# Optimization experiments

Measured on AMD Instinct MI355X. Metric: run time of the kernel, lower is better.

The kernel has to match this reference:

```python
import jax, jax.numpy as jnp
import numpy as np

N = 50000        # nodes
E = 800000       # edges (avg degree 16)
HIDDEN = 256
HEADS = 8
HEAD_DIM = HIDDEN // HEADS


def _linear_params(key, fan_in, fan_out):
    k1, k2 = jax.random.split(key)
    s = 1.0 / np.sqrt(fan_in)
    W = jax.random.uniform(k1, (fan_in, fan_out), jnp.float32, -s, s)
    b = jax.random.uniform(k2, (fan_out,), jnp.float32, -s, s)
    return W, b


def setup_inputs() -> dict:
    key = jax.random.key(0)
    ks = jax.random.split(key, 7)
    h = jax.random.normal(ks[0], (N, HIDDEN), jnp.float32)
    # sparse adjacency nonzeros: row = destination node, col = source node
    row = jnp.sort(jax.random.randint(ks[1], (E,), 0, N))
    col = jax.random.randint(ks[2], (E,), 0, N)
    Wq, bq = _linear_params(ks[3], HIDDEN, HIDDEN)
    Wk, bk = _linear_params(ks[4], HIDDEN, HIDDEN)
    Wv, bv = _linear_params(ks[5], HIDDEN, HIDDEN)
    Wo, bo = _linear_params(ks[6], HIDDEN, HIDDEN)
    return dict(h=h, row=row, col=col, Wq=Wq, bq=bq, Wk=Wk, bk=bk,
                Wv=Wv, bv=bv, Wo=Wo, bo=bo)


def reference(h, row, col, Wq, bq, Wk, bk, Wv, bv, Wo, bo):
    n = h.shape[0]
    scaling = HEAD_DIM ** (-0.5)
    q = ((h @ Wq + bq).reshape(n, HEADS, HEAD_DIM)) * scaling
    k = (h @ Wk + bk).reshape(n, HEADS, HEAD_DIM)
    v = (h @ Wv + bv).reshape(n, HEADS, HEAD_DIM)

    # bsddmm: per-edge, per-head sampled dot product q[dst] . k[src] -> [E, H]
    s = jnp.einsum('ehd,ehd->eh', q[row], k[col])

    # sparse row-wise softmax over each destination node's incoming edges
    m = jax.ops.segment_max(s, row, num_segments=n)          # [N, H]
    p = jnp.exp(s - m[row])                                   # [E, H]
    denom = jax.ops.segment_sum(p, row, num_segments=n)      # [N, H]
    attn = p / denom[row]                                     # [E, H]

    # bspmm: out[dst] = sum over incoming edges attn * v[src] -> [N, H, D]
    out = jax.ops.segment_sum(attn[:, :, None] * v[col], row, num_segments=n)
    return out.reshape(n, HIDDEN) @ Wo + bo
```

## Files before the change

### kernel.cpp

```cpp
#include <hip/hip_runtime.h>
#include <math.h>


typedef __attribute__((ext_vector_type(8))) short bf16x8;
typedef __attribute__((ext_vector_type(4))) float f32x4;
typedef __attribute__((ext_vector_type(2))) float f32x2;

__device__ __forceinline__ ushort f2bf(float f) {
    uint u = __float_as_uint(f);
    u += 0x7fffu + ((u >> 16) & 1u);
    return (ushort)(u >> 16);
}
__device__ __forceinline__ float bflo(uint u) { return __uint_as_float(u << 16); }
__device__ __forceinline__ float bfhi(uint u) { return __uint_as_float(u & 0xffff0000u); }

__device__ __forceinline__ uchar f2fp8(float f) {
    return (uchar)(__builtin_amdgcn_cvt_pk_fp8_f32(f, f, 0, false) & 0xff);
}
__device__ __forceinline__ void fp8x4_to_f32(uint u, float* f) {
    f32x2 lo = __builtin_amdgcn_cvt_pk_f32_fp8(u, false);
    f32x2 hi = __builtin_amdgcn_cvt_pk_f32_fp8(u, true);
    f[0] = lo[0]; f[1] = lo[1]; f[2] = hi[0]; f[3] = hi[1];
}

__device__ __forceinline__ void load_lds16(const void* g, void* l) {
    __builtin_amdgcn_global_load_lds(
        (const __attribute__((address_space(1))) void*)g,
        (__attribute__((address_space(3))) void*)l, 16, 0, 0);
}

__global__ __launch_bounds__(256) void convert_bf16(
    const float* __restrict__ in, ushort* __restrict__ out, size_t nelem)
{
    size_t i = ((size_t)blockIdx.x * 256 + threadIdx.x) * 4;
    if (i >= nelem) return;
    float4 v = *(const float4*)(in + i);
    *(ushort4*)(out + i) = make_ushort4(f2bf(v.x), f2bf(v.y), f2bf(v.z), f2bf(v.w));
}

__global__ __launch_bounds__(256) void prep_w(
    const float* __restrict__ Wq, const float* __restrict__ Wk,
    const float* __restrict__ Wv, const float* __restrict__ Wo,
    const float* __restrict__ bq, const float* __restrict__ bk,
    const float* __restrict__ bv,
    ushort* __restrict__ Wall, ushort* __restrict__ Wot,
    float* __restrict__ ball)
{
    int m = blockIdx.y;
    if (blockIdx.x < 256) {
        int idx = blockIdx.x * 256 + threadIdx.x;
        int k = idx >> 8, nn = idx & 255;
        if (m < 3) {
            const float* W = m == 0 ? Wq : (m == 1 ? Wk : Wv);
            Wall[((size_t)m * 256 + nn) * 256 + k] = f2bf(W[idx]);
        } else {
            Wot[nn * 256 + k] = f2bf(Wo[idx]);
        }
    } else if (m < 3) {
        int i = threadIdx.x;
        ball[m * 256 + i] = (m == 0 ? bq : (m == 1 ? bk : bv))[i];
    }
}

template<int MODE>
__global__ __launch_bounds__(256) void gemm_mfma_lds(
    const ushort* __restrict__ A, const ushort* __restrict__ Wt,
    const float* __restrict__ bias, ushort* __restrict__ qb,
    uchar* __restrict__ kv, float* __restrict__ outf, int n, float scale)
{
    __shared__ ushort SH[2 * 128 * 64];
    ushort* As = SH;
    ushort* Bs = SH + 128 * 64;

    const int nwg = gridDim.x * gridDim.y;
    const int orig = blockIdx.y * gridDim.x + blockIdx.x;
    const int xcd = orig & 7, rnd = orig >> 3;
    const int q8 = nwg >> 3, r8 = nwg & 7;
    const int wgid = (xcd < r8 ? xcd * (q8 + 1) : r8 * (q8 + 1) + (xcd - r8) * q8) + rnd;
    const int tx = wgid % gridDim.x;
    const int ty = wgid / gridDim.x;

    const int tid = threadIdx.x;
    const int lane = tid & 63;
    const int wave = tid >> 6;
    const int col0 = tx * 128;
    const int row0 = ty * 128;
    const int fr = lane & 15;
    const int kg = lane >> 4;
    const int wr = (wave >> 1) * 64;
    const int wc = (wave & 1) * 64;

    f32x4 acc[4][4] = {};

    const int srow = tid >> 3;
    const int sc8 = tid & 7;

    for (int kt = 0; kt < 4; ++kt) {
        #pragma unroll
        for (int it = 0; it < 4; ++it) {
            int r = srow + it * 32;
            int chunk = sc8 ^ (r & 7);
            int ar = row0 + r; ar = ar < n ? ar : n - 1;
            load_lds16((const char*)A + (size_t)ar * 512 + kt * 128 + chunk * 16,
                       (char*)As + (it * 256 + tid) * 16);
            load_lds16((const char*)Wt + (size_t)(col0 + r) * 512 + kt * 128 + chunk * 16,
                       (char*)Bs + (it * 256 + tid) * 16);
        }
        __syncthreads();

        #pragma unroll
        for (int ks = 0; ks < 2; ++ks) {
            bf16x8 a[4], b[4];
            #pragma unroll
            for (int i = 0; i < 4; ++i) {
                int r = wr + i * 16 + fr;
                int chunk = (ks * 4 + kg) ^ (r & 7);
                a[i] = *(const bf16x8*)((const char*)As + r * 128 + chunk * 16);
            }
            #pragma unroll
            for (int j = 0; j < 4; ++j) {
                int c = wc + j * 16 + fr;
                int chunk = (ks * 4 + kg) ^ (c & 7);
                b[j] = *(const bf16x8*)((const char*)Bs + c * 128 + chunk * 16);
            }
            #pragma unroll
            for (int i = 0; i < 4; ++i)
                #pragma unroll
                for (int j = 0; j < 4; ++j)
                    acc[i][j] = __builtin_amdgcn_mfma_f32_16x16x32_bf16(
                        a[i], b[j], acc[i][j], 0, 0, 0);
        }
        __syncthreads();
    }

    if constexpr (MODE == 1) {
        #pragma unroll
        for (int j = 0; j < 4; ++j) {
            int gcol = col0 + wc + j * 16 + fr;
            float bj = bias[gcol];
            #pragma unroll
            for (int i = 0; i < 4; ++i) {
                #pragma unroll
                for (int r = 0; r < 4; ++r) {
                    int grow = row0 + wr + i * 16 + kg * 4 + r;
                    if (grow >= n) continue;
                    outf[(size_t)grow * 256 + gcol] = acc[i][j][r] + bj;
                }
            }
        }
        return;
    }

    char* sb = (char*)SH;
    const bool isf8 = (col0 >= 256 && col0 < 512);
    const float sc = (col0 < 256) ? scale : 1.f;

    #pragma unroll
    for (int j = 0; j < 4; ++j) {
        int cw = wc + j * 16 + fr;
        float bj = bias[col0 + cw];
        #pragma unroll
        for (int i = 0; i < 4; ++i) {
            #pragma unroll
            for (int r = 0; r < 4; ++r) {
                int lrow = wr + i * 16 + kg * 4 + r;
                float val = (acc[i][j][r] + bj) * sc;
                if (isf8) {
                    int u = cw >> 4;
                    sb[lrow * 128 + ((u ^ (lrow & 7)) << 4) + (cw & 15)] = f2fp8(val);
                } else {
                    int u = cw >> 3;
                    *(ushort*)(sb + lrow * 256 + ((u ^ (lrow & 7)) << 4) +
                               ((cw & 7) << 1)) = f2bf(val);
                }
            }
        }
    }
    __syncthreads();

    if (isf8) {
        int seg = col0 - 256;
        #pragma unroll
        for (int pass = 0; pass < 4; ++pass) {
            int g = pass * 256 + tid;
            int lrow = g >> 3, u = g & 7;
            uint4 d = *(const uint4*)(sb + lrow * 128 + ((u ^ (lrow & 7)) << 4));
            int grow = row0 + lrow;
            if (grow < n)
                *(uint4*)((char*)kv + (size_t)grow * 768 + seg + u * 16) = d;
        }
    } else {
        char* dst; size_t stride; int seg;
        if (col0 < 256) { dst = (char*)qb; stride = 512; seg = col0 * 2; }
        else            { dst = (char*)kv; stride = 768; seg = 256 + (col0 - 512) * 2; }
        #pragma unroll
        for (int pass = 0; pass < 8; ++pass) {
            int g = pass * 256 + tid;
            int lrow = g >> 4, u = g & 15;
            uint4 d = *(const uint4*)(sb + lrow * 256 + ((u ^ (lrow & 7)) << 4));
            int grow = row0 + lrow;
            if (grow < n)
                *(uint4*)(dst + (size_t)grow * stride + seg + u * 16) = d;
        }
    }
}

__global__ __launch_bounds__(256) void build_row_ptr(
    const int* __restrict__ row, int* __restrict__ row_ptr, int n, int E)
{
    int i = blockIdx.x * 256 + threadIdx.x;
    if (i > n) return;
    int lo = 0, hi = E;
    while (lo < hi) {
        int mid = (lo + hi) >> 1;
        if (row[mid] < i) lo = mid + 1; else hi = mid;
    }
    row_ptr[i] = lo;
}

__global__ __launch_bounds__(256) void fused_attn(
    const ushort* __restrict__ qb, const uchar* __restrict__ kv,
    const int* __restrict__ col, const int* __restrict__ row_ptr,
    ushort* __restrict__ agg, int n)
{
    int node = blockIdx.x * 4 + (threadIdx.x >> 6);
    if (node >= n) return;
    int lane = threadIdx.x & 63;
    int p0 = row_ptr[node], p1 = row_ptr[node + 1];

    const int slot = lane >> 4;
    const int l16 = lane & 15;
    const int qoff = l16 * 32;

    float qf[16];
    {
        const char* qbp = (const char*)qb + (size_t)node * 512 + qoff;
        uint4 q0 = *(const uint4*)qbp;
        uint4 q1 = *(const uint4*)(qbp + 16);
        qf[0] = bflo(q0.x); qf[1] = bfhi(q0.x);
        qf[2] = bflo(q0.y); qf[3] = bfhi(q0.y);
        qf[4] = bflo(q0.z); qf[5] = bfhi(q0.z);
        qf[6] = bflo(q0.w); qf[7] = bfhi(q0.w);
        qf[8] = bflo(q1.x); qf[9] = bfhi(q1.x);
        qf[10] = bflo(q1.y); qf[11] = bfhi(q1.y);
        qf[12] = bflo(q1.z); qf[13] = bfhi(q1.z);
        qf[14] = bflo(q1.w); qf[15] = bfhi(q1.w);
    }

    float denom = 0.f;
    float acc[16] = {};

#define ISSUE(IDX, K, V0, V1)                                                  \
    do {                                                                       \
        int src_ = __shfl(cl, (IDX));                                          \
        const char* b_ = (const char*)kv + (size_t)src_ * 768;                 \
        K  = *(const uint4*)(b_ + l16 * 16);                                   \
        V0 = *(const uint4*)(b_ + 256 + l16 * 32);                             \
        V1 = *(const uint4*)(b_ + 272 + l16 * 32);                             \
    } while (0)

#define CONSUME(VALID, K, V0, V1)                                              \
    do {                                                                       \
        float kf_[16];                                                         \
        fp8x4_to_f32(K.x, kf_); fp8x4_to_f32(K.y, kf_ + 4);                    \
        fp8x4_to_f32(K.z, kf_ + 8); fp8x4_to_f32(K.w, kf_ + 12);               \
        float sp_ = 0.f;                                                       \
        _Pragma("unroll")                                                      \
        for (int i_ = 0; i_ < 16; ++i_) sp_ = fmaf(qf[i_], kf_[i_], sp_);      \
        float s_ = sp_ + __shfl_xor(sp_, 1);                                   \
        float p_ = (VALID) ? __expf(s_) : 0.f;                                 \
        denom += p_;                                                           \
        acc[0]  = fmaf(p_, bflo(V0.x), acc[0]);                                \
        acc[1]  = fmaf(p_, bfhi(V0.x), acc[1]);                                \
        acc[2]  = fmaf(p_, bflo(V0.y), acc[2]);                                \
        acc[3]  = fmaf(p_, bfhi(V0.y), acc[3]);                                \
        acc[4]  = fmaf(p_, bflo(V0.z), acc[4]);                                \
        acc[5]  = fmaf(p_, bfhi(V0.z), acc[5]);                                \
        acc[6]  = fmaf(p_, bflo(V0.w), acc[6]);                                \
        acc[7]  = fmaf(p_, bfhi(V0.w), acc[7]);                                \
        acc[8]  = fmaf(p_, bflo(V1.x), acc[8]);                                \
        acc[9]  = fmaf(p_, bfhi(V1.x), acc[9]);                                \
        acc[10] = fmaf(p_, bflo(V1.y), acc[10]);                               \
        acc[11] = fmaf(p_, bfhi(V1.y), acc[11]);                               \
        acc[12] = fmaf(p_, bflo(V1.z), acc[12]);                               \
        acc[13] = fmaf(p_, bfhi(V1.z), acc[13]);                               \
        acc[14] = fmaf(p_, bflo(V1.w), acc[14]);                               \
        acc[15] = fmaf(p_, bfhi(V1.w), acc[15]);                               \
    } while (0)

    for (int bbase = p0; bbase < p1; bbase += 64) {
        int bd = min(64, p1 - bbase);
        int cl = (lane < bd) ? col[bbase + lane] : 0;
        int nch = (bd + 3) >> 2;

        uint4 kA, vA0, vA1, kB, vB0, vB1;
        ISSUE(slot, kA, vA0, vA1);
        int c = 0;
        for (;;) {
            if (c + 1 < nch) ISSUE((c + 1) * 4 + slot, kB, vB0, vB1);
            CONSUME(c * 4 + slot < bd, kA, vA0, vA1);
            if (++c >= nch) break;
            if (c + 1 < nch) ISSUE((c + 1) * 4 + slot, kA, vA0, vA1);
            CONSUME(c * 4 + slot < bd, kB, vB0, vB1);
            if (++c >= nch) break;
        }
    }
#undef ISSUE
#undef CONSUME

    #pragma unroll
    for (int i = 0; i < 16; ++i) {
        acc[i] += __shfl_xor(acc[i], 16);
        acc[i] += __shfl_xor(acc[i], 32);
    }
    denom += __shfl_xor(denom, 16);
    denom += __shfl_xor(denom, 32);

    if (slot == 0) {
        float inv = denom > 0.f ? 1.f / denom : 0.f;
        uint o[8];
        #pragma unroll
        for (int i = 0; i < 8; ++i)
            o[i] = (uint)f2bf(acc[2 * i] * inv) |
                   ((uint)f2bf(acc[2 * i + 1] * inv) << 16);
        char* ob = (char*)agg + (size_t)node * 512 + qoff;
        *(uint4*)ob        = make_uint4(o[0], o[1], o[2], o[3]);
        *(uint4*)(ob + 16) = make_uint4(o[4], o[5], o[6], o[7]);
    }
}

extern "C" void kernel_launch(void* const* d_in, const int* in_sizes, int n_in,
                              void* d_out, int out_size, void* d_ws, size_t ws_size,
                              hipStream_t stream)
{
    const float* h  = (const float*)d_in[0];
    const int*   row = (const int*)d_in[1];
    const int*   col = (const int*)d_in[2];
    const float* Wq = (const float*)d_in[3];
    const float* bq = (const float*)d_in[4];
    const float* Wk = (const float*)d_in[5];
    const float* bk = (const float*)d_in[6];
    const float* Wv = (const float*)d_in[7];
    const float* bv = (const float*)d_in[8];
    const float* Wo = (const float*)d_in[9];
    const float* bo = (const float*)d_in[10];
    float* out = (float*)d_out;

    const int n = in_sizes[0] / 256;
    const int E = in_sizes[1];
    const size_t NC = (size_t)n * 256;

    char* base = (char*)d_ws;
    ushort* qbb  = (ushort*)(base);
    uchar*  kv   = (uchar*)(base + NC * 2);
    ushort* hb   = (ushort*)(base + NC * 2 + (size_t)n * 768);
    ushort* aggb = (ushort*)(base + NC * 4 + (size_t)n * 768);
    ushort* Wall = (ushort*)(base + NC * 6 + (size_t)n * 768);
    ushort* Wot  = Wall + 768 * 256;
    float*  ball = (float*)(Wot + 65536);
    int* row_ptr = (int*)(ball + 768);

    const float scaling = 0.17677669529663687f;

    dim3 blk(256);
    convert_bf16<<<dim3((int)((NC / 4 + 255) / 256)), blk, 0, stream>>>(h, hb, NC);
    prep_w<<<dim3(257, 4), blk, 0, stream>>>(Wq, Wk, Wv, Wo, bq, bk, bv,
                                             Wall, Wot, ball);
    build_row_ptr<<<dim3((n + 256) / 256), blk, 0, stream>>>(row, row_ptr, n, E);

    const int mtiles = (n + 127) / 128;
    gemm_mfma_lds<0><<<dim3(6, mtiles), blk, 0, stream>>>(
        hb, Wall, ball, qbb, kv, nullptr, n, scaling);

    fused_attn<<<dim3((n + 3) / 4), blk, 0, stream>>>(
        qbb, kv, col, row_ptr, aggb, n);

    gemm_mfma_lds<1><<<dim3(2, mtiles), blk, 0, stream>>>(
        aggb, Wot, bo, nullptr, nullptr, out, n, 1.f);
}
```

Before: 175.7 us.

## Fuse fp32-to-bf16 conversion into QKV GEMM with resident A tile, merge prep launches

The QKV projection now loads h as fp32 directly, converts it to bf16 into a swizzled LDS tile covering the full K dimension for 64 rows, and loops over all six output column tiles inside one block. This removes the separate conversion kernel and its intermediate bf16 buffer round trip through memory. The row_ptr binary search is folded into the weight prep kernel as an extra grid row, saving a launch. In exchange there are fewer, heavier blocks with larger LDS use, and no double buffering of the weight tiles.

```diff
diff --git a/kernel.cpp b/kernel.cpp
--- a/kernel.cpp
+++ b/kernel.cpp
@@ -29,24 +29,27 @@
         (__attribute__((address_space(3))) void*)l, 16, 0, 0);
 }
 
-__global__ __launch_bounds__(256) void convert_bf16(
-    const float* __restrict__ in, ushort* __restrict__ out, size_t nelem)
-{
-    size_t i = ((size_t)blockIdx.x * 256 + threadIdx.x) * 4;
-    if (i >= nelem) return;
-    float4 v = *(const float4*)(in + i);
-    *(ushort4*)(out + i) = make_ushort4(f2bf(v.x), f2bf(v.y), f2bf(v.z), f2bf(v.w));
-}
-
-__global__ __launch_bounds__(256) void prep_w(
+__global__ __launch_bounds__(256) void prep(
     const float* __restrict__ Wq, const float* __restrict__ Wk,
     const float* __restrict__ Wv, const float* __restrict__ Wo,
     const float* __restrict__ bq, const float* __restrict__ bk,
     const float* __restrict__ bv,
+    const int* __restrict__ row, int* __restrict__ row_ptr, int n, int E,
     ushort* __restrict__ Wall, ushort* __restrict__ Wot,
     float* __restrict__ ball)
 {
     int m = blockIdx.y;
+    if (m == 4) {
+        int i = blockIdx.x * 256 + threadIdx.x;
+        if (i > n) return;
+        int lo = 0, hi = E;
+        while (lo < hi) {
+            int mid = (lo + hi) >> 1;
+            if (row[mid] < i) lo = mid + 1; else hi = mid;
+        }
+        row_ptr[i] = lo;
+        return;
+    }
     if (blockIdx.x < 256) {
         int idx = blockIdx.x * 256 + threadIdx.x;
         int k = idx >> 8, nn = idx & 255;
@@ -62,15 +65,139 @@
     }
 }
 
-template<int MODE>
-__global__ __launch_bounds__(256) void gemm_mfma_lds(
+__global__ __launch_bounds__(256) void gemm_qkv(
+    const float* __restrict__ h, const ushort* __restrict__ Wall,
+    const float* __restrict__ ball, ushort* __restrict__ qb,
+    uchar* __restrict__ kv, int n, float scale)
+{
+    __shared__ ushort As[64 * 256];
+    __shared__ ushort Bs[128 * 64];
+
+    const int tid = threadIdx.x;
+    const int lane = tid & 63;
+    const int wave = tid >> 6;
+    const int row0 = blockIdx.x * 64;
+
+    #pragma unroll 4
+    for (int j = 0; j < 16; ++j) {
+        int r = j * 4 + wave;
+        int src_r = row0 + r; if (src_r >= n) src_r = n - 1;
+        float4 f = *(const float4*)((const char*)h + (size_t)src_r * 1024 + lane * 16);
+        uint lo = (uint)f2bf(f.x) | ((uint)f2bf(f.y) << 16);
+        uint hi = (uint)f2bf(f.z) | ((uint)f2bf(f.w) << 16);
+        int addr = r * 512 + (((lane >> 1) ^ (r & 7)) << 4) + ((lane & 1) << 3);
+        *(uint2*)((char*)As + addr) = make_uint2(lo, hi);
+    }
+
+    const int fr = lane & 15;
+    const int kg = lane >> 4;
+    const int wr = (wave >> 1) * 32;
+    const int wc = (wave & 1) * 64;
+
+    for (int ct = 0; ct < 6; ++ct) {
+        f32x4 acc[2][4] = {};
+
+        for (int kt = 0; kt < 4; ++kt) {
+            #pragma unroll
+            for (int it = 0; it < 4; ++it) {
+                int r = (tid >> 3) + it * 32;
+                int chunk = (tid & 7) ^ (r & 7);
+                load_lds16((const char*)Wall + (size_t)(ct * 128 + r) * 512 +
+                               kt * 128 + chunk * 16,
+                           (char*)Bs + (it * 256 + tid) * 16);
+            }
+            __syncthreads();
+
+            #pragma unroll
+            for (int ks = 0; ks < 2; ++ks) {
+                bf16x8 a[2], b[4];
+                #pragma unroll
+                for (int i = 0; i < 2; ++i) {
+                    int r = wr + i * 16 + fr;
+                    int c16 = kt * 8 + ks * 4 + kg;
+                    a[i] = *(const bf16x8*)((const char*)As + r * 512 +
+                                            ((c16 ^ (r & 7)) << 4));
+                }
+                #pragma unroll
+                for (int jj = 0; jj < 4; ++jj) {
+                    int rb = wc + jj * 16 + fr;
+                    int chunk = (ks * 4 + kg) ^ (rb & 7);
+                    b[jj] = *(const bf16x8*)((const char*)Bs + rb * 128 + chunk * 16);
+                }
+                #pragma unroll
+                for (int i = 0; i < 2; ++i)
+                    #pragma unroll
+                    for (int jj = 0; jj < 4; ++jj)
+                        acc[i][jj] = __builtin_amdgcn_mfma_f32_16x16x32_bf16(
+                            a[i], b[jj], acc[i][jj], 0, 0, 0);
+            }
+            __syncthreads();
+        }
+
+        const bool isf8 = (ct == 2 || ct == 3);
+        const float sc = (ct < 2) ? scale : 1.f;
+        char* sb = (char*)Bs;
+
+        #pragma unroll
+        for (int jj = 0; jj < 4; ++jj) {
+            int cw = wc + jj * 16 + fr;
+            float bj = ball[ct * 128 + cw];
+            #pragma unroll
+            for (int i = 0; i < 2; ++i) {
+                #pragma unroll
+                for (int r2 = 0; r2 < 4; ++r2) {
+                    int lrow = wr + i * 16 + kg * 4 + r2;
+                    float val = (acc[i][jj][r2] + bj) * sc;
+                    if (isf8) {
+                        int u = cw >> 4;
+                        sb[lrow * 128 + ((u ^ (lrow & 7)) << 4) + (cw & 15)] =
+                            f2fp8(val);
+                    } else {
+                        int u = cw >> 3;
+                        *(ushort*)(sb + lrow * 256 + ((u ^ (lrow & 7)) << 4) +
+                                   ((cw & 7) << 1)) = f2bf(val);
+                    }
+                }
+            }
+        }
+        __syncthreads();
+
+        if (isf8) {
+            #pragma unroll
+            for (int cp = 0; cp < 2; ++cp) {
+                int g = cp * 256 + tid;
+                int lrow = g >> 3, u = g & 7;
+                uint4 d = *(const uint4*)(sb + lrow * 128 + ((u ^ (lrow & 7)) << 4));
+                int grow = row0 + lrow;
+                if (grow < n)
+                    *(uint4*)((char*)kv + (size_t)grow * 768 + (ct - 2) * 128 +
+                              u * 16) = d;
+            }
+        } else {
+            #pragma unroll
+            for (int cp = 0; cp < 4; ++cp) {
+                int g = cp * 256 + tid;
+                int lrow = g >> 4, u = g & 15;
+                uint4 d = *(const uint4*)(sb + lrow * 256 + ((u ^ (lrow & 7)) << 4));
+                int grow = row0 + lrow;
+                if (grow >= n) continue;
+                if (ct < 2)
+                    *(uint4*)((char*)qb + (size_t)grow * 512 + ct * 256 + u * 16) = d;
+                else
+                    *(uint4*)((char*)kv + (size_t)grow * 768 + 256 +
+                              (ct - 4) * 256 + u * 16) = d;
+            }
+        }
+        __syncthreads();
+    }
+}
+
+__global__ __launch_bounds__(256) void gemm_out(
     const ushort* __restrict__ A, const ushort* __restrict__ Wt,
-    const float* __restrict__ bias, ushort* __restrict__ qb,
-    uchar* __restrict__ kv, float* __restrict__ outf, int n, float scale)
+    const float* __restrict__ bias, float* __restrict__ outf, int n)
 {
-    __shared__ ushort SH[2 * 128 * 64];
-    ushort* As = SH;
-    ushort* Bs = SH + 128 * 64;
+    __shared__ ushort As[128 * 64];
+    __shared__ ushort Bs[128 * 64];
 
     const int nwg = gridDim.x * gridDim.y;
     const int orig = blockIdx.y * gridDim.x + blockIdx.x;
@@ -133,89 +260,20 @@
         __syncthreads();
     }
 
-    if constexpr (MODE == 1) {
-        #pragma unroll
-        for (int j = 0; j < 4; ++j) {
-            int gcol = col0 + wc + j * 16 + fr;
-            float bj = bias[gcol];
-            #pragma unroll
-            for (int i = 0; i < 4; ++i) {
-                #pragma unroll
-                for (int r = 0; r < 4; ++r) {
-                    int grow = row0 + wr + i * 16 + kg * 4 + r;
-                    if (grow >= n) continue;
-                    outf[(size_t)grow * 256 + gcol] = acc[i][j][r] + bj;
-                }
-            }
-        }
-        return;
-    }
-
-    char* sb = (char*)SH;
-    const bool isf8 = (col0 >= 256 && col0 < 512);
-    const float sc = (col0 < 256) ? scale : 1.f;
-
     #pragma unroll
     for (int j = 0; j < 4; ++j) {
-        int cw = wc + j * 16 + fr;
-        float bj = bias[col0 + cw];
+        int gcol = col0 + wc + j * 16 + fr;
+        float bj = bias[gcol];
         #pragma unroll
         for (int i = 0; i < 4; ++i) {
             #pragma unroll
             for (int r = 0; r < 4; ++r) {
-                int lrow = wr + i * 16 + kg * 4 + r;
-                float val = (acc[i][j][r] + bj) * sc;
-                if (isf8) {
-                    int u = cw >> 4;
-                    sb[lrow * 128 + ((u ^ (lrow & 7)) << 4) + (cw & 15)] = f2fp8(val);
-                } else {
-                    int u = cw >> 3;
-                    *(ushort*)(sb + lrow * 256 + ((u ^ (lrow & 7)) << 4) +
-                               ((cw & 7) << 1)) = f2bf(val);
-                }
-            }
-        }
-    }
-    __syncthreads();
-
-    if (isf8) {
-        int seg = col0 - 256;
-        #pragma unroll
-        for (int pass = 0; pass < 4; ++pass) {
-            int g = pass * 256 + tid;
-            int lrow = g >> 3, u = g & 7;
-            uint4 d = *(const uint4*)(sb + lrow * 128 + ((u ^ (lrow & 7)) << 4));
-            int grow = row0 + lrow;
-            if (grow < n)
-                *(uint4*)((char*)kv + (size_t)grow * 768 + seg + u * 16) = d;
-        }
-    } else {
-        char* dst; size_t stride; int seg;
-        if (col0 < 256) { dst = (char*)qb; stride = 512; seg = col0 * 2; }
-        else            { dst = (char*)kv; stride = 768; seg = 256 + (col0 - 512) * 2; }
-        #pragma unroll
-        for (int pass = 0; pass < 8; ++pass) {
-            int g = pass * 256 + tid;
-            int lrow = g >> 4, u = g & 15;
-            uint4 d = *(const uint4*)(sb + lrow * 256 + ((u ^ (lrow & 7)) << 4));
-            int grow = row0 + lrow;
-            if (grow < n)
-                *(uint4*)(dst + (size_t)grow * stride + seg + u * 16) = d;
-        }
-    }
-}
-
-__global__ __launch_bounds__(256) void build_row_ptr(
-    const int* __restrict__ row, int* __restrict__ row_ptr, int n, int E)
-{
-    int i = blockIdx.x * 256 + threadIdx.x;
-    if (i > n) return;
-    int lo = 0, hi = E;
-    while (lo < hi) {
-        int mid = (lo + hi) >> 1;
-        if (row[mid] < i) lo = mid + 1; else hi = mid;
-    }
-    row_ptr[i] = lo;
+                int grow = row0 + wr + i * 16 + kg * 4 + r;
+                if (grow >= n) continue;
+                outf[(size_t)grow * 256 + gcol] = acc[i][j][r] + bj;
+            }
+        }
+    }
 }
 
 __global__ __launch_bounds__(256) void fused_attn(
@@ -353,9 +411,8 @@
     char* base = (char*)d_ws;
     ushort* qbb  = (ushort*)(base);
     uchar*  kv   = (uchar*)(base + NC * 2);
-    ushort* hb   = (ushort*)(base + NC * 2 + (size_t)n * 768);
-    ushort* aggb = (ushort*)(base + NC * 4 + (size_t)n * 768);
-    ushort* Wall = (ushort*)(base + NC * 6 + (size_t)n * 768);
+    ushort* aggb = (ushort*)(base + NC * 2 + (size_t)n * 768);
+    ushort* Wall = (ushort*)(base + NC * 4 + (size_t)n * 768);
     ushort* Wot  = Wall + 768 * 256;
     float*  ball = (float*)(Wot + 65536);
     int* row_ptr = (int*)(ball + 768);
@@ -363,18 +420,16 @@
     const float scaling = 0.17677669529663687f;
 
     dim3 blk(256);
-    convert_bf16<<<dim3((int)((NC / 4 + 255) / 256)), blk, 0, stream>>>(h, hb, NC);
-    prep_w<<<dim3(257, 4), blk, 0, stream>>>(Wq, Wk, Wv, Wo, bq, bk, bv,
-                                             Wall, Wot, ball);
-    build_row_ptr<<<dim3((n + 256) / 256), blk, 0, stream>>>(row, row_ptr, n, E);
-
-    const int mtiles = (n + 127) / 128;
-    gemm_mfma_lds<0><<<dim3(6, mtiles), blk, 0, stream>>>(
-        hb, Wall, ball, qbb, kv, nullptr, n, scaling);
+    prep<<<dim3(257, 5), blk, 0, stream>>>(Wq, Wk, Wv, Wo, bq, bk, bv,
+                                           row, row_ptr, n, E,
+                                           Wall, Wot, ball);
+
+    gemm_qkv<<<dim3((n + 63) / 64), blk, 0, stream>>>(
+        h, Wall, ball, qbb, kv, n, scaling);
 
     fused_attn<<<dim3((n + 3) / 4), blk, 0, stream>>>(
         qbb, kv, col, row_ptr, aggb, n);
 
-    gemm_mfma_lds<1><<<dim3(2, mtiles), blk, 0, stream>>>(
-        aggb, Wot, bo, nullptr, nullptr, out, n, 1.f);
-}
+    gemm_out<<<dim3(2, (n + 127) / 128), blk, 0, stream>>>(
+        aggb, Wot, bo, out, n);
+}
```

New measurement: 178.8 us. About the same (+1.7%).

## Quantize V to per-head int8 with scales and merge row_ptr build into prep

Applied to the files above, without the earlier changes.

Stores V as unsigned 8-bit values with a per-node, per-head float scale (absmax/127, offset 128) instead of bf16. The per-row K/V record in the gathered buffer shrinks from 768 to 544 bytes. The attention kernel gathers one 16-byte V load plus a scale per edge, accumulates on the offset bytes, and corrects the offset at the end with a running sum. The row_ptr binary search is also folded into the weight-prep kernel to save one launch. The lower V precision adds accuracy risk and a few extra conversion ALU ops per edge.

```diff
diff --git a/kernel.cpp b/kernel.cpp
--- a/kernel.cpp
+++ b/kernel.cpp
@@ -38,15 +38,27 @@
     *(ushort4*)(out + i) = make_ushort4(f2bf(v.x), f2bf(v.y), f2bf(v.z), f2bf(v.w));
 }
 
-__global__ __launch_bounds__(256) void prep_w(
+__global__ __launch_bounds__(256) void prep(
     const float* __restrict__ Wq, const float* __restrict__ Wk,
     const float* __restrict__ Wv, const float* __restrict__ Wo,
     const float* __restrict__ bq, const float* __restrict__ bk,
     const float* __restrict__ bv,
+    const int* __restrict__ row, int* __restrict__ row_ptr, int n, int E,
     ushort* __restrict__ Wall, ushort* __restrict__ Wot,
     float* __restrict__ ball)
 {
     int m = blockIdx.y;
+    if (m == 4) {
+        int i = blockIdx.x * 256 + threadIdx.x;
+        if (i > n) return;
+        int lo = 0, hi = E;
+        while (lo < hi) {
+            int mid = (lo + hi) >> 1;
+            if (row[mid] < i) lo = mid + 1; else hi = mid;
+        }
+        row_ptr[i] = lo;
+        return;
+    }
     if (blockIdx.x < 256) {
         int idx = blockIdx.x * 256 + threadIdx.x;
         int k = idx >> 8, nn = idx & 255;
@@ -153,6 +165,7 @@
 
     char* sb = (char*)SH;
     const bool isf8 = (col0 >= 256 && col0 < 512);
+    const bool isv  = (col0 >= 512);
     const float sc = (col0 < 256) ? scale : 1.f;
 
     #pragma unroll
@@ -162,9 +175,9 @@
         #pragma unroll
         for (int i = 0; i < 4; ++i) {
             #pragma unroll
-            for (int r = 0; r < 4; ++r) {
-                int lrow = wr + i * 16 + kg * 4 + r;
-                float val = (acc[i][j][r] + bj) * sc;
+            for (int r2 = 0; r2 < 4; ++r2) {
+                int lrow = wr + i * 16 + kg * 4 + r2;
+                float val = (acc[i][j][r2] + bj) * sc;
                 if (isf8) {
                     int u = cw >> 4;
                     sb[lrow * 128 + ((u ^ (lrow & 7)) << 4) + (cw & 15)] = f2fp8(val);
@@ -187,12 +200,48 @@
             uint4 d = *(const uint4*)(sb + lrow * 128 + ((u ^ (lrow & 7)) << 4));
             int grow = row0 + lrow;
             if (grow < n)
-                *(uint4*)((char*)kv + (size_t)grow * 768 + seg + u * 16) = d;
+                *(uint4*)((char*)kv + (size_t)grow * 544 + seg + u * 16) = d;
+        }
+    } else if (isv) {
+        int vseg = col0 - 512;
+        #pragma unroll
+        for (int pass = 0; pass < 2; ++pass) {
+            int t = pass * 256 + tid;
+            int lrow = t >> 2, hh = t & 3;
+            float vals[32];
+            #pragma unroll
+            for (int uu = 0; uu < 4; ++uu) {
+                int u = hh * 4 + uu;
+                uint4 d = *(const uint4*)(sb + lrow * 256 + ((u ^ (lrow & 7)) << 4));
+                vals[uu*8+0] = bflo(d.x); vals[uu*8+1] = bfhi(d.x);
+                vals[uu*8+2] = bflo(d.y); vals[uu*8+3] = bfhi(d.y);
+                vals[uu*8+4] = bflo(d.z); vals[uu*8+5] = bfhi(d.z);
+                vals[uu*8+6] = bflo(d.w); vals[uu*8+7] = bfhi(d.w);
+            }
+            float mx = 0.f;
+            #pragma unroll
+            for (int i = 0; i < 32; ++i) mx = fmaxf(mx, fabsf(vals[i]));
+            float inv = mx > 0.f ? 127.f / mx : 0.f;
+            float scl = mx > 0.f ? mx * (1.f / 127.f) : 0.f;
+            uint pk[8];
+            #pragma unroll
+            for (int w = 0; w < 8; ++w) {
+                uint b0 = (uint)(__float2int_rn(vals[w*4+0] * inv) + 128);
+                uint b1 = (uint)(__float2int_rn(vals[w*4+1] * inv) + 128);
+                uint b2 = (uint)(__float2int_rn(vals[w*4+2] * inv) + 128);
+                uint b3 = (uint)(__float2int_rn(vals[w*4+3] * inv) + 128);
+                pk[w] = b0 | (b1 << 8) | (b2 << 16) | (b3 << 24);
+            }
+            int grow = row0 + lrow;
+            if (grow < n) {
+                char* dst = (char*)kv + (size_t)grow * 544 + 256 + vseg + hh * 32;
+                *(uint4*)dst        = make_uint4(pk[0], pk[1], pk[2], pk[3]);
+                *(uint4*)(dst + 16) = make_uint4(pk[4], pk[5], pk[6], pk[7]);
+                *(float*)((char*)kv + (size_t)grow * 544 + 512 +
+                          ((vseg >> 5) + hh) * 4) = scl;
+            }
         }
     } else {
-        char* dst; size_t stride; int seg;
-        if (col0 < 256) { dst = (char*)qb; stride = 512; seg = col0 * 2; }
-        else            { dst = (char*)kv; stride = 768; seg = 256 + (col0 - 512) * 2; }
         #pragma unroll
         for (int pass = 0; pass < 8; ++pass) {
             int g = pass * 256 + tid;
@@ -200,22 +249,9 @@
             uint4 d = *(const uint4*)(sb + lrow * 256 + ((u ^ (lrow & 7)) << 4));
             int grow = row0 + lrow;
             if (grow < n)
-                *(uint4*)(dst + (size_t)grow * stride + seg + u * 16) = d;
-        }
-    }
-}
-
-__global__ __launch_bounds__(256) void build_row_ptr(
-    const int* __restrict__ row, int* __restrict__ row_ptr, int n, int E)
-{
-    int i = blockIdx.x * 256 + threadIdx.x;
-    if (i > n) return;
-    int lo = 0, hi = E;
-    while (lo < hi) {
-        int mid = (lo + hi) >> 1;
-        if (row[mid] < i) lo = mid + 1; else hi = mid;
-    }
-    row_ptr[i] = lo;
+                *(uint4*)((char*)qb + (size_t)grow * 512 + col0 * 2 + u * 16) = d;
+        }
+    }
 }
 
 __global__ __launch_bounds__(256) void fused_attn(
@@ -248,18 +284,19 @@
     }
 
     float denom = 0.f;
+    float cacc = 0.f;
     float acc[16] = {};
 
-#define ISSUE(IDX, K, V0, V1)                                                  \
+#define ISSUE(IDX, K, V, S)                                                    \
     do {                                                                       \
         int src_ = __shfl(cl, (IDX));                                          \
-        const char* b_ = (const char*)kv + (size_t)src_ * 768;                 \
-        K  = *(const uint4*)(b_ + l16 * 16);                                   \
-        V0 = *(const uint4*)(b_ + 256 + l16 * 32);                             \
-        V1 = *(const uint4*)(b_ + 272 + l16 * 32);                             \
+        const char* b_ = (const char*)kv + (size_t)src_ * 544;                 \
+        K = *(const uint4*)(b_ + l16 * 16);                                    \
+        V = *(const uint4*)(b_ + 256 + l16 * 16);                              \
+        S = *(const float*)(b_ + 512 + ((l16 >> 1) << 2));                     \
     } while (0)
 
-#define CONSUME(VALID, K, V0, V1)                                              \
+#define CONSUME(VALID, K, V, S)                                                \
     do {                                                                       \
         float kf_[16];                                                         \
         fp8x4_to_f32(K.x, kf_); fp8x4_to_f32(K.y, kf_ + 4);                    \
@@ -270,22 +307,29 @@
         float s_ = sp_ + __shfl_xor(sp_, 1);                                   \
         float p_ = (VALID) ? __expf(s_) : 0.f;                                 \
         denom += p_;                                                           \
-        acc[0]  = fmaf(p_, bflo(V0.x), acc[0]);                                \
-        acc[1]  = fmaf(p_, bfhi(V0.x), acc[1]);                                \
-        acc[2]  = fmaf(p_, bflo(V0.y), acc[2]);                                \
-        acc[3]  = fmaf(p_, bfhi(V0.y), acc[3]);                                \
-        acc[4]  = fmaf(p_, bflo(V0.z), acc[4]);                                \
-        acc[5]  = fmaf(p_, bfhi(V0.z), acc[5]);                                \
-        acc[6]  = fmaf(p_, bflo(V0.w), acc[6]);                                \
-        acc[7]  = fmaf(p_, bfhi(V0.w), acc[7]);                                \
-        acc[8]  = fmaf(p_, bflo(V1.x), acc[8]);                                \
-        acc[9]  = fmaf(p_, bfhi(V1.x), acc[9]);                                \
-        acc[10] = fmaf(p_, bflo(V1.y), acc[10]);                               \
-        acc[11] = fmaf(p_, bfhi(V1.y), acc[11]);                               \
-        acc[12] = fmaf(p_, bflo(V1.z), acc[12]);                               \
-        acc[13] = fmaf(p_, bfhi(V1.z), acc[13]);                               \
-        acc[14] = fmaf(p_, bflo(V1.w), acc[14]);                               \
-        acc[15] = fmaf(p_, bfhi(V1.w), acc[15]);                               \
+        float ps_ = p_ * (S);                                                  \
+        cacc += ps_;                                                           \
+        uint w_;                                                               \
+        w_ = V.x;                                                              \
+        acc[0]  = fmaf(ps_, (float)(w_ & 0xff),         acc[0]);               \
+        acc[1]  = fmaf(ps_, (float)((w_ >> 8) & 0xff),  acc[1]);               \
+        acc[2]  = fmaf(ps_, (float)((w_ >> 16) & 0xff), acc[2]);               \
+        acc[3]  = fmaf(ps_, (float)(w_ >> 24),          acc[3]);               \
+        w_ = V.y;                                                              \
+        acc[4]  = fmaf(ps_, (float)(w_ & 0xff),         acc[4]);               \
+        acc[5]  = fmaf(ps_, (float)((w_ >> 8) & 0xff),  acc[5]);               \
+        acc[6]  = fmaf(ps_, (float)((w_ >> 16) & 0xff), acc[6]);               \
+        acc[7]  = fmaf(ps_, (float)(w_ >> 24),          acc[7]);               \
+        w_ = V.z;                                                              \
+        acc[8]  = fmaf(ps_, (float)(w_ & 0xff),         acc[8]);               \
+        acc[9]  = fmaf(ps_, (float)((w_ >> 8) & 0xff),  acc[9]);               \
+        acc[10] = fmaf(ps_, (float)((w_ >> 16) & 0xff), acc[10]);              \
+        acc[11] = fmaf(ps_, (float)(w_ >> 24),          acc[11]);              \
+        w_ = V.w;                                                              \
+        acc[12] = fmaf(ps_, (float)(w_ & 0xff),         acc[12]);              \
+        acc[13] = fmaf(ps_, (float)((w_ >> 8) & 0xff),  acc[13]);              \
+        acc[14] = fmaf(ps_, (float)((w_ >> 16) & 0xff), acc[14]);              \
+        acc[15] = fmaf(ps_, (float)(w_ >> 24),          acc[15]);              \
     } while (0)
 
     for (int bbase = p0; bbase < p1; bbase += 64) {
@@ -293,21 +337,23 @@
         int cl = (lane < bd) ? col[bbase + lane] : 0;
         int nch = (bd + 3) >> 2;
 
-        uint4 kA, vA0, vA1, kB, vB0, vB1;
-        ISSUE(slot, kA, vA0, vA1);
+        uint4 kA, vA, kB, vB; float sA, sB;
+        ISSUE(slot, kA, vA, sA);
         int c = 0;
         for (;;) {
-            if (c + 1 < nch) ISSUE((c + 1) * 4 + slot, kB, vB0, vB1);
-            CONSUME(c * 4 + slot < bd, kA, vA0, vA1);
+            if (c + 1 < nch) ISSUE((c + 1) * 4 + slot, kB, vB, sB);
+            CONSUME(c * 4 + slot < bd, kA, vA, sA);
             if (++c >= nch) break;
-            if (c + 1 < nch) ISSUE((c + 1) * 4 + slot, kA, vA0, vA1);
-            CONSUME(c * 4 + slot < bd, kB, vB0, vB1);
+            if (c + 1 < nch) ISSUE((c + 1) * 4 + slot, kA, vA, sA);
+            CONSUME(c * 4 + slot < bd, kB, vB, sB);
             if (++c >= nch) break;
         }
     }
 #undef ISSUE
 #undef CONSUME
 
+    #pragma unroll
+    for (int i = 0; i < 16; ++i) acc[i] = fmaf(-128.f, cacc, acc[i]);
     #pragma unroll
     for (int i = 0; i < 16; ++i) {
         acc[i] += __shfl_xor(acc[i], 16);
@@ -353,9 +399,10 @@
     char* base = (char*)d_ws;
     ushort* qbb  = (ushort*)(base);
     uchar*  kv   = (uchar*)(base + NC * 2);
-    ushort* hb   = (ushort*)(base + NC * 2 + (size_t)n * 768);
-    ushort* aggb = (ushort*)(base + NC * 4 + (size_t)n * 768);
-    ushort* Wall = (ushort*)(base + NC * 6 + (size_t)n * 768);
+    char*   p2   = base + NC * 2 + (size_t)n * 544;
+    ushort* hb   = (ushort*)(p2);
+    ushort* aggb = (ushort*)(p2 + NC * 2);
+    ushort* Wall = (ushort*)(p2 + NC * 4);
     ushort* Wot  = Wall + 768 * 256;
     float*  ball = (float*)(Wot + 65536);
     int* row_ptr = (int*)(ball + 768);
@@ -363,10 +410,10 @@
     const float scaling = 0.17677669529663687f;
 
     dim3 blk(256);
+    prep<<<dim3(257, 5), blk, 0, stream>>>(Wq, Wk, Wv, Wo, bq, bk, bv,
+                                           row, row_ptr, n, E,
+                                           Wall, Wot, ball);
     convert_bf16<<<dim3((int)((NC / 4 + 255) / 256)), blk, 0, stream>>>(h, hb, NC);
-    prep_w<<<dim3(257, 4), blk, 0, stream>>>(Wq, Wk, Wv, Wo, bq, bk, bv,
-                                             Wall, Wot, ball);
-    build_row_ptr<<<dim3((n + 256) / 256), blk, 0, stream>>>(row, row_ptr, n, E);
 
     const int mtiles = (n + 127) / 128;
     gemm_mfma_lds<0><<<dim3(6, mtiles), blk, 0, stream>>>(
```

After: 158.9 us. 1.11x faster.
